# Optimization experiments

Measured on AMD Instinct MI355X. Metric: run time of the kernel, lower is better.

Reference implementation:

```python
import jax, jax.numpy as jnp
import numpy as np

N_SRC = 50000
N_DST = 50000
N_EDGE = 800000
D_SRC = 128
D_DST = 128
D_EDGE = D_SRC + 2 + D_DST  # 258


def setup_inputs() -> dict:
    key = jax.random.key(0)
    ks = jax.random.split(key, 7)
    return {
        "src_node_features": jax.random.normal(ks[0], (N_SRC, D_SRC), jnp.float32),
        "edge_src_idx": jax.random.randint(ks[1], (N_EDGE,), 0, N_SRC, dtype=jnp.int32),
        "dst_node_features": jax.random.normal(ks[2], (N_DST, D_DST), jnp.float32),
        "edge_dst_idx": jax.random.randint(ks[3], (N_EDGE,), 0, N_DST, dtype=jnp.int32),
        "edge_dist_rel": jax.random.normal(ks[4], (N_EDGE, 2), jnp.float32),
        # nn.Linear(258, 1, bias=False) weight stored as a [258] vector
        "w_att": jax.random.normal(ks[5], (D_EDGE,), jnp.float32) * 0.05,
        # nn.Linear(258, 128, bias=False) weight stored transposed [258, 128]
        "w_embed": jax.random.normal(ks[6], (D_EDGE, D_DST), jnp.float32) * 0.05,
    }


def reference(src_node_features, edge_src_idx, dst_node_features, edge_dst_idx,
              edge_dist_rel, w_att, w_embed):
    # Gather endpoint features per edge and concat with relative distance: [E, 258]
    x = jnp.concatenate([
        src_node_features[edge_src_idx],
        edge_dist_rel,
        dst_node_features[edge_dst_idx],
    ], axis=-1)

    # Edge attention score: Linear(258->1, no bias) + LeakyReLU(0.2)
    score = x @ w_att                                     # [E]
    score = jnp.where(score >= 0, score, 0.2 * score)

    # scatter_softmax over destination segments (numerically stable)
    seg_max = jax.ops.segment_max(score, edge_dst_idx, num_segments=N_DST)
    seg_max = jnp.where(jnp.isfinite(seg_max), seg_max, 0.0)  # empty segments
    e = jnp.exp(score - seg_max[edge_dst_idx])
    denom = jax.ops.segment_sum(e, edge_dst_idx, num_segments=N_DST)
    attn = e / denom[edge_dst_idx]                        # [E]
    # Dropout is identity in eval mode.

    # Edge embedding and attention-weighted scatter_add: [N_DST, 128]
    emb = x @ w_embed                                     # [E, 128]
    out = jax.ops.segment_sum(attn[:, None] * emb, edge_dst_idx, num_segments=N_DST)
    return jax.nn.relu(out)
```

## Files before the change

kernel.cpp:

```cpp
#include <hip/hip_runtime.h>
#include <hip/hip_bf16.h>

#define D 128
#define NPB 64
#define EPB1 2048
#define BDST 32
#define CAP 1024
#define MAXBINS 2048
#define NCHUNK 8

typedef __attribute__((ext_vector_type(8))) short short8;
typedef __attribute__((ext_vector_type(4))) float f32x4;

static __device__ __forceinline__ unsigned short f32_to_bf16(float f) {
    unsigned int u = __float_as_uint(f);
    u = (u + 0x7FFFu + ((u >> 16) & 1u)) >> 16;
    return (unsigned short)u;
}
static __device__ __forceinline__ float bf16lo(unsigned int r) {
    return __uint_as_float(r << 16);
}
static __device__ __forceinline__ float bf16hi(unsigned int r) {
    return __uint_as_float(r & 0xFFFF0000u);
}

__global__ void __launch_bounds__(256)
wconv_kernel(const float* __restrict__ w_embed, unsigned short* __restrict__ w_frag)
{
    int t = blockIdx.x * 256 + threadIdx.x;
    if (t >= 4096) return;
    int set  = t >> 11;
    int ks   = (t >> 9) & 3;
    int nt   = (t >> 6) & 7;
    int lane = t & 63;
    int wrow0 = set ? 130 : 0;
    int col   = nt * 16 + (lane & 15);
    int kbase = ks * 32 + (lane >> 4) * 8;
    unsigned short* dst = w_frag + (size_t)t * 8;
#pragma unroll
    for (int j = 0; j < 8; ++j)
        dst[j] = f32_to_bf16(w_embed[(size_t)(wrow0 + kbase + j) * D + col]);
}

__global__ void __launch_bounds__(256)
proj_both_kernel(const float* __restrict__ src_feat, const float* __restrict__ dst_feat,
                 const unsigned short* __restrict__ wfrag_base,
                 const float* __restrict__ w_att,
                 int n_src, int n_dst, int nblk_src,
                 unsigned short* __restrict__ srcp, unsigned short* __restrict__ dstp,
                 float* __restrict__ src_att, float* __restrict__ dst_att)
{
    const bool is_src = (blockIdx.x < nblk_src);
    const float* feats = is_src ? src_feat : dst_feat;
    const unsigned short* wfrag = is_src ? wfrag_base : wfrag_base + 16384;
    const int wrow = is_src ? 0 : 130;
    const int n_nodes = is_src ? n_src : n_dst;
    unsigned short* proj = is_src ? srcp : dstp;
    float* att = is_src ? src_att : dst_att;
    const int blk = is_src ? blockIdx.x : blockIdx.x - nblk_src;

    __shared__ unsigned short s_tile[NPB * D];
    __shared__ float s_red[NPB][4];

    const int tid = threadIdx.x;
    const int node0 = blk * NPB;

#pragma unroll
    for (int it = 0; it < 8; ++it) {
        int idx = it * 256 + tid;
        int row = idx >> 5, c4 = idx & 31;
        int n = node0 + row;
        float4 v = (n < n_nodes)
                 ? *reinterpret_cast<const float4*>(&feats[(size_t)n * D + c4 * 4])
                 : make_float4(0.f, 0.f, 0.f, 0.f);
        unsigned short h[4];
        h[0] = f32_to_bf16(v.x); h[1] = f32_to_bf16(v.y);
        h[2] = f32_to_bf16(v.z); h[3] = f32_to_bf16(v.w);
        int byte = row * 256 + c4 * 8;
        byte ^= (row & 7) << 4;
        *reinterpret_cast<ushort4*>((char*)s_tile + byte) = *reinterpret_cast<ushort4*>(h);
    }
    __syncthreads();

    const int wv = tid >> 6, lane = tid & 63;

    f32x4 acc[8];
#pragma unroll
    for (int i = 0; i < 8; ++i) acc[i] = {0.f, 0.f, 0.f, 0.f};

    const int arow = wv * 16 + (lane & 15);
#pragma unroll
    for (int ks = 0; ks < 4; ++ks) {
        int abyte = arow * 256 + ks * 64 + (lane >> 4) * 16;
        abyte ^= (arow & 7) << 4;
        short8 a = *reinterpret_cast<const short8*>((char*)s_tile + abyte);
#pragma unroll
        for (int nt = 0; nt < 8; ++nt) {
            short8 b = *reinterpret_cast<const short8*>(wfrag + ((size_t)(ks * 8 + nt) * 64 + lane) * 8);
            acc[nt] = __builtin_amdgcn_mfma_f32_16x16x32_bf16(a, b, acc[nt], 0, 0, 0);
        }
    }

#pragma unroll
    for (int nt = 0; nt < 8; ++nt) {
#pragma unroll
        for (int r = 0; r < 4; ++r) {
            int node = node0 + wv * 16 + (lane >> 4) * 4 + r;
            if (node < n_nodes)
                proj[(size_t)node * D + nt * 16 + (lane & 15)] = f32_to_bf16(acc[nt][r]);
        }
    }

    const int na = tid & 63, kq = tid >> 6;
    float p = 0.f;
#pragma unroll
    for (int k = kq * 32; k < kq * 32 + 32; ++k) {
        int byte = (na * 256 + k * 2) ^ ((na & 7) << 4);
        unsigned short h = *reinterpret_cast<const unsigned short*>((char*)s_tile + byte);
        p += __uint_as_float(((unsigned int)h) << 16) * w_att[wrow + k];
    }
    s_red[na][kq] = p;
    __syncthreads();
    if (tid < NPB) {
        int n = node0 + tid;
        if (n < n_nodes)
            att[n] = s_red[tid][0] + s_red[tid][1] + s_red[tid][2] + s_red[tid][3];
    }
}

__global__ void __launch_bounds__(512)
hist1_kernel(const int* __restrict__ edst, int* __restrict__ bb,
             int n_edge, int nblk1, int nb1)
{
    __shared__ int bins[MAXBINS];
    const int tid = threadIdx.x, blk = blockIdx.x;
    for (int i = tid; i < nb1; i += 512) bins[i] = 0;
    __syncthreads();
    const int e0 = blk * EPB1 + tid * 4;
    if (e0 + 4 <= n_edge) {
        int4 d4 = *reinterpret_cast<const int4*>(&edst[e0]);
        atomicAdd(&bins[((unsigned)d4.x) >> 5], 1);
        atomicAdd(&bins[((unsigned)d4.y) >> 5], 1);
        atomicAdd(&bins[((unsigned)d4.z) >> 5], 1);
        atomicAdd(&bins[((unsigned)d4.w) >> 5], 1);
    } else {
        for (int e = e0; e < n_edge; ++e)
            atomicAdd(&bins[((unsigned)edst[e]) >> 5], 1);
    }
    __syncthreads();
    for (int i = tid; i < nb1; i += 512) bb[(size_t)blk * nb1 + i] = bins[i];
}

__global__ void __launch_bounds__(256)
chunksum_kernel(const int* __restrict__ bb, int* __restrict__ cs,
                int nb1, int nblk1, int cb)
{
    int t = blockIdx.x * 256 + threadIdx.x;
    if (t >= nb1 * NCHUNK) return;
    int c = t / nb1, bin = t - c * nb1;
    int b0 = c * cb, b1 = min(b0 + cb, nblk1);
    int s = 0;
    for (int blk = b0; blk < b1; ++blk)
        s += bb[(size_t)blk * nb1 + bin];
    cs[(size_t)c * nb1 + bin] = s;
}

__global__ void __launch_bounds__(1024)
midscan_kernel(int* __restrict__ cs, int* __restrict__ binstart,
               int nb1, int n_edge)
{
    __shared__ int s_tot[MAXBINS];
    __shared__ int s_w[16];
    __shared__ int s_total;
    __shared__ int s_carry;
    const int tid = threadIdx.x;
    const int lane = tid & 63, wid = tid >> 6;

    for (int bin = tid; bin < nb1; bin += 1024) {
        int run = 0;
#pragma unroll
        for (int c = 0; c < NCHUNK; ++c) {
            size_t idx = (size_t)c * nb1 + bin;
            int v = cs[idx];
            cs[idx] = run;
            run += v;
        }
        s_tot[bin] = run;
    }
    if (tid == 0) s_carry = 0;
    __syncthreads();

    for (int base = 0; base < nb1; base += 1024) {
        int idx = base + tid;
        int v = (idx < nb1) ? s_tot[idx] : 0;
        int x = v;
#pragma unroll
        for (int off = 1; off < 64; off <<= 1) {
            int y = __shfl_up(x, off);
            if (lane >= off) x += y;
        }
        if (lane == 63) s_w[wid] = x;
        __syncthreads();
        if (tid < 16) {
            int w = s_w[tid];
            int xi = w;
#pragma unroll
            for (int off = 1; off < 16; off <<= 1) {
                int y = __shfl_up(xi, off);
                if (tid >= off) xi += y;
            }
            if (tid == 15) s_total = xi;
            s_w[tid] = xi - w;
        }
        __syncthreads();
        if (idx < nb1) binstart[idx] = s_carry + s_w[wid] + (x - v);
        __syncthreads();
        if (tid == 0) s_carry += s_total;
        __syncthreads();
    }
    if (tid == 0) binstart[nb1] = n_edge;
}

__global__ void __launch_bounds__(256)
chunkwrite_kernel(int* __restrict__ bb, const int* __restrict__ cs,
                  int nb1, int nblk1, int cb)
{
    int t = blockIdx.x * 256 + threadIdx.x;
    if (t >= nb1 * NCHUNK) return;
    int c = t / nb1, bin = t - c * nb1;
    int b0 = c * cb, b1 = min(b0 + cb, nblk1);
    int carry = cs[(size_t)c * nb1 + bin];
    for (int blk0 = b0; blk0 < b1; blk0 += 8) {
        int v[8];
#pragma unroll
        for (int j = 0; j < 8; ++j) {
            int blk = blk0 + j;
            v[j] = (blk < b1) ? bb[(size_t)blk * nb1 + bin] : 0;
        }
#pragma unroll
        for (int j = 0; j < 8; ++j) {
            int blk = blk0 + j;
            if (blk < b1) bb[(size_t)blk * nb1 + bin] = carry;
            carry += v[j];
        }
    }
}

__global__ void __launch_bounds__(512)
pass1_kernel(const int* __restrict__ esrc, const int* __restrict__ edst,
             const float* __restrict__ dist,
             const float* __restrict__ src_att, const float* __restrict__ dst_att,
             const float* __restrict__ w_att,
             const int* __restrict__ bb, const int* __restrict__ binstart,
             float4* __restrict__ meta1, int n_edge, int nblk1, int nb1)
{
    __shared__ int cur[MAXBINS];
    const int tid = threadIdx.x, blk = blockIdx.x;
    for (int i = tid; i < nb1; i += 512)
        cur[i] = binstart[i] + bb[(size_t)blk * nb1 + i];
    __syncthreads();

    const float wa0 = w_att[128], wa1 = w_att[129];
    const int e0 = blk * EPB1 + tid * 4;
    if (e0 + 4 <= n_edge) {
        int4 s4 = *reinterpret_cast<const int4*>(&esrc[e0]);
        int4 d4 = *reinterpret_cast<const int4*>(&edst[e0]);
        float4 da = *reinterpret_cast<const float4*>(&dist[2 * (size_t)e0]);
        float4 db = *reinterpret_cast<const float4*>(&dist[2 * (size_t)e0 + 4]);
        float sa0 = src_att[s4.x], sa1 = src_att[s4.y];
        float sa2 = src_att[s4.z], sa3 = src_att[s4.w];
        float ta0 = dst_att[d4.x], ta1 = dst_att[d4.y];
        float ta2 = dst_att[d4.z], ta3 = dst_att[d4.w];
        float c0 = sa0 + ta0 + da.x * wa0 + da.y * wa1;
        float c1 = sa1 + ta1 + da.z * wa0 + da.w * wa1;
        float c2 = sa2 + ta2 + db.x * wa0 + db.y * wa1;
        float c3 = sa3 + ta3 + db.z * wa0 + db.w * wa1;
        c0 = (c0 >= 0.f) ? c0 : 0.2f * c0;
        c1 = (c1 >= 0.f) ? c1 : 0.2f * c1;
        c2 = (c2 >= 0.f) ? c2 : 0.2f * c2;
        c3 = (c3 >= 0.f) ? c3 : 0.2f * c3;
        float w0 = __expf(c0), w1 = __expf(c1), w2 = __expf(c2), w3 = __expf(c3);
        int p0 = atomicAdd(&cur[((unsigned)d4.x) >> 5], 1);
        int p1 = atomicAdd(&cur[((unsigned)d4.y) >> 5], 1);
        int p2 = atomicAdd(&cur[((unsigned)d4.z) >> 5], 1);
        int p3 = atomicAdd(&cur[((unsigned)d4.w) >> 5], 1);
        meta1[p0] = make_float4(__int_as_float(s4.x | ((d4.x & 31) << 24)), w0, da.x, da.y);
        meta1[p1] = make_float4(__int_as_float(s4.y | ((d4.y & 31) << 24)), w1, da.z, da.w);
        meta1[p2] = make_float4(__int_as_float(s4.z | ((d4.z & 31) << 24)), w2, db.x, db.y);
        meta1[p3] = make_float4(__int_as_float(s4.w | ((d4.w & 31) << 24)), w3, db.z, db.w);
    } else {
        for (int e = e0; e < n_edge; ++e) {
            int s = esrc[e];
            int d = edst[e];
            float2 dd = *reinterpret_cast<const float2*>(&dist[2 * (size_t)e]);
            float sc = src_att[s] + dst_att[d] + dd.x * wa0 + dd.y * wa1;
            sc = (sc >= 0.f) ? sc : 0.2f * sc;
            float ew = __expf(sc);
            int pos = atomicAdd(&cur[((unsigned)d) >> 5], 1);
            meta1[pos] = make_float4(__int_as_float(s | ((d & 31) << 24)), ew, dd.x, dd.y);
        }
    }
}

__global__ void __launch_bounds__(256)
p2agg_kernel(const float4* __restrict__ meta1, const int* __restrict__ binstart,
             const unsigned short* __restrict__ srcp,
             const unsigned short* __restrict__ dstp,
             const float* __restrict__ w_embed,
             float* __restrict__ out, int n_dst)
{
    __shared__ float4 s_meta[CAP];
    __shared__ int s_cnt[BDST];
    __shared__ int s_ofs[BDST + 1];
    __shared__ int s_cur[BDST];

    const int tid = threadIdx.x;
    const int b = blockIdx.x;
    const int bstart = binstart[b], bend = binstart[b + 1];
    const int bsize = bend - bstart;
    const int lane = tid & 63, wv = tid >> 6;
    const int c0 = 2 * lane;

    const float2 wd0 = *reinterpret_cast<const float2*>(&w_embed[128 * D + c0]);
    const float2 wd1 = *reinterpret_cast<const float2*>(&w_embed[129 * D + c0]);

    if (tid < BDST) s_cnt[tid] = 0;
    __syncthreads();

    if (bsize <= CAP) {
        for (int i = tid; i < bsize; i += 256) {
            int bits = __float_as_int(meta1[bstart + i].x);
            atomicAdd(&s_cnt[((unsigned)bits) >> 24], 1);
        }
        __syncthreads();
        if (tid < BDST) {
            int v = s_cnt[tid];
            int x = v;
#pragma unroll
            for (int off = 1; off < BDST; off <<= 1) {
                int y = __shfl_up(x, off);
                if (tid >= off) x += y;
            }
            s_ofs[tid] = x - v;
            s_cur[tid] = x - v;
            if (tid == BDST - 1) s_ofs[BDST] = x;
        }
        __syncthreads();
        for (int i = tid; i < bsize; i += 256) {
            float4 m = meta1[bstart + i];
            int dlow = ((unsigned)__float_as_int(m.x)) >> 24;
            int pos = atomicAdd(&s_cur[dlow], 1);
            s_meta[pos] = m;
        }
        __syncthreads();

#define EDGE_ACC(m)                                                               \
        {                                                                         \
            int bits_ = __float_as_int((m).x);                                    \
            unsigned int r_ = *reinterpret_cast<const unsigned int*>(             \
                &srcp[(size_t)(bits_ & 0xFFFFFF) * D + c0]);                      \
            acc0 += (m).y * bf16lo(r_);                                           \
            acc1 += (m).y * bf16hi(r_);                                           \
            sw   += (m).y;                                                        \
            swd0 += (m).y * (m).z;                                                \
            swd1 += (m).y * (m).w;                                                \
        }
#pragma unroll
        for (int k = 0; k < 8; ++k) {
            int dloc = k * 4 + wv;
            int gd = b * BDST + dloc;
            if (gd >= n_dst) continue;
            float2* op = reinterpret_cast<float2*>(&out[(size_t)gd * D + c0]);
            int o0 = s_ofs[dloc], o1 = s_ofs[dloc + 1];
            if (o0 == o1) { *op = make_float2(0.f, 0.f); continue; }

            float acc0 = 0.f, acc1 = 0.f, sw = 0.f, swd0 = 0.f, swd1 = 0.f;
            int j = o0;
            for (; j + 8 <= o1; j += 8) {
                float4 m0 = s_meta[j + 0];
                float4 m1 = s_meta[j + 1];
                float4 m2 = s_meta[j + 2];
                float4 m3 = s_meta[j + 3];
                float4 m4 = s_meta[j + 4];
                float4 m5 = s_meta[j + 5];
                float4 m6 = s_meta[j + 6];
                float4 m7 = s_meta[j + 7];
                EDGE_ACC(m0) EDGE_ACC(m1) EDGE_ACC(m2) EDGE_ACC(m3)
                EDGE_ACC(m4) EDGE_ACC(m5) EDGE_ACC(m6) EDGE_ACC(m7)
            }
            for (; j < o1; ++j) {
                float4 m0 = s_meta[j];
                EDGE_ACC(m0)
            }
            float inv = 1.f / sw;
            unsigned int rd = *reinterpret_cast<const unsigned int*>(&dstp[(size_t)gd * D + c0]);
            float ov0 = (acc0 + swd0 * wd0.x + swd1 * wd1.x) * inv + bf16lo(rd);
            float ov1 = (acc1 + swd0 * wd0.y + swd1 * wd1.y) * inv + bf16hi(rd);
            *op = make_float2(fmaxf(ov0, 0.f), fmaxf(ov1, 0.f));
        }
#undef EDGE_ACC
    } else {
        float acc0[8], acc1[8], sw[8], s0[8], s1[8];
        for (int k = 0; k < 8; ++k) { acc0[k] = acc1[k] = sw[k] = s0[k] = s1[k] = 0.f; }
        for (int cs2 = bstart; cs2 < bend; cs2 += CAP) {
            int n = min(CAP, bend - cs2);
            __syncthreads();
            for (int i = tid; i < n; i += 256) s_meta[i] = meta1[cs2 + i];
            __syncthreads();
            for (int k = 0; k < 8; ++k) {
                int dloc = k * 4 + wv;
                for (int i = 0; i < n; ++i) {
                    float4 m = s_meta[i];
                    int bits = __float_as_int(m.x);
                    if ((int)(((unsigned)bits) >> 24) == dloc) {
                        unsigned int r = *reinterpret_cast<const unsigned int*>(
                            &srcp[(size_t)(bits & 0xFFFFFF) * D + c0]);
                        acc0[k] += m.y * bf16lo(r);
                        acc1[k] += m.y * bf16hi(r);
                        sw[k] += m.y;
                        s0[k] += m.y * m.z;
                        s1[k] += m.y * m.w;
                    }
                }
            }
        }
        for (int k = 0; k < 8; ++k) {
            int dloc = k * 4 + wv;
            int gd = b * BDST + dloc;
            if (gd >= n_dst) continue;
            float2* op = reinterpret_cast<float2*>(&out[(size_t)gd * D + c0]);
            if (sw[k] == 0.f) { *op = make_float2(0.f, 0.f); continue; }
            float inv = 1.f / sw[k];
            unsigned int rd = *reinterpret_cast<const unsigned int*>(&dstp[(size_t)gd * D + c0]);
            float ov0 = (acc0[k] + s0[k] * wd0.x + s1[k] * wd1.x) * inv + bf16lo(rd);
            float ov1 = (acc1[k] + s0[k] * wd0.y + s1[k] * wd1.y) * inv + bf16hi(rd);
            *op = make_float2(fmaxf(ov0, 0.f), fmaxf(ov1, 0.f));
        }
    }
}

extern "C" void kernel_launch(void* const* d_in, const int* in_sizes, int n_in,
                              void* d_out, int out_size, void* d_ws, size_t ws_size,
                              hipStream_t stream)
{
    const float* src_feat = (const float*)d_in[0];
    const int*   esrc     = (const int*)d_in[1];
    const float* dst_feat = (const float*)d_in[2];
    const int*   edst     = (const int*)d_in[3];
    const float* dist     = (const float*)d_in[4];
    const float* w_att    = (const float*)d_in[5];
    const float* w_embed  = (const float*)d_in[6];

    const int n_src  = in_sizes[0] / D;
    const int n_edge = in_sizes[1];
    const int n_dst  = in_sizes[2] / D;

    const int nb1   = (n_dst + BDST - 1) / BDST;
    const int nblk1 = (n_edge + EPB1 - 1) / EPB1;
    const int cb    = (nblk1 + NCHUNK - 1) / NCHUNK;
    const size_t n1 = (size_t)nb1 * nblk1;

    char* p = (char*)d_ws;
    auto carve = [&p](size_t bytes) {
        char* r = p;
        p += (bytes + 255) & ~size_t(255);
        return r;
    };
    unsigned short* src_projb = (unsigned short*)carve((size_t)n_src * D * 2);
    unsigned short* dst_projb = (unsigned short*)carve((size_t)n_dst * D * 2);
    float* src_att   = (float*)carve((size_t)n_src * 4);
    float* dst_att   = (float*)carve((size_t)n_dst * 4);
    int*   bb        = (int*)carve(n1 * 4);
    int*   cs        = (int*)carve((size_t)NCHUNK * nb1 * 4);
    int*   binstart  = (int*)carve((size_t)(nb1 + 1) * 4);
    unsigned short* w_frag = (unsigned short*)carve(2 * 4 * 8 * 64 * 8 * 2);
    float4* meta1    = (float4*)carve((size_t)n_edge * 16);
    (void)ws_size;

    wconv_kernel<<<16, 256, 0, stream>>>(w_embed, w_frag);

    const int nblk_src = (n_src + NPB - 1) / NPB;
    const int nblk_dst = (n_dst + NPB - 1) / NPB;
    proj_both_kernel<<<nblk_src + nblk_dst, 256, 0, stream>>>(
        src_feat, dst_feat, w_frag, w_att, n_src, n_dst, nblk_src,
        src_projb, dst_projb, src_att, dst_att);

    hist1_kernel<<<nblk1, 512, 0, stream>>>(edst, bb, n_edge, nblk1, nb1);

    const int nthr_cs = nb1 * NCHUNK;
    chunksum_kernel<<<(nthr_cs + 255) / 256, 256, 0, stream>>>(bb, cs, nb1, nblk1, cb);
    midscan_kernel<<<1, 1024, 0, stream>>>(cs, binstart, nb1, n_edge);
    chunkwrite_kernel<<<(nthr_cs + 255) / 256, 256, 0, stream>>>(bb, cs, nb1, nblk1, cb);

    pass1_kernel<<<nblk1, 512, 0, stream>>>(esrc, edst, dist, src_att, dst_att,
                                            w_att, bb, binstart, meta1,
                                            n_edge, nblk1, nb1);

    p2agg_kernel<<<nb1, 256, 0, stream>>>(meta1, binstart, src_projb, dst_projb,
                                          w_embed, (float*)d_out, n_dst);
}
```

Measured before the change: 113.9 us.

## Stage gathered source rows in LDS chunks with cooperative 16-byte loads

The aggregation kernel now cooperatively gathers chunks of 64 source-feature rows into shared memory using 16-byte loads per thread, then each wave accumulates its destinations from LDS. The per-destination weight sums are computed up front with a wave-parallel reduction instead of serially per edge. This is meant to replace per-lane 4-byte scattered global loads with wider coalesced loads. In exchange it adds a block-wide barrier per chunk, extra LDS use that may lower occupancy, and serial per-destination loops over each chunk that leave most waves idle when few of their edges fall in a chunk.

```diff
diff --git a/kernel.cpp b/kernel.cpp
--- a/kernel.cpp
+++ b/kernel.cpp
@@ -8,6 +8,7 @@
 #define CAP 1024
 #define MAXBINS 2048
 #define NCHUNK 8
+#define NC 64
 
 typedef __attribute__((ext_vector_type(8))) short short8;
 typedef __attribute__((ext_vector_type(4))) float f32x4;
@@ -310,6 +311,7 @@
              float* __restrict__ out, int n_dst)
 {
     __shared__ float4 s_meta[CAP];
+    __shared__ unsigned short s_rows[NC * D];
     __shared__ int s_cnt[BDST];
     __shared__ int s_ofs[BDST + 1];
     __shared__ int s_cur[BDST];
@@ -354,51 +356,69 @@
         }
         __syncthreads();
 
-#define EDGE_ACC(m)                                                               \
-        {                                                                         \
-            int bits_ = __float_as_int((m).x);                                    \
-            unsigned int r_ = *reinterpret_cast<const unsigned int*>(             \
-                &srcp[(size_t)(bits_ & 0xFFFFFF) * D + c0]);                      \
-            acc0 += (m).y * bf16lo(r_);                                           \
-            acc1 += (m).y * bf16hi(r_);                                           \
-            sw   += (m).y;                                                        \
-            swd0 += (m).y * (m).z;                                                \
-            swd1 += (m).y * (m).w;                                                \
-        }
+        int o0[8], o1[8];
+        float sw[8], sd0[8], sd1[8];
+#pragma unroll
+        for (int k = 0; k < 8; ++k) {
+            int dloc = k * 4 + wv;
+            o0[k] = s_ofs[dloc];
+            o1[k] = s_ofs[dloc + 1];
+            float a = 0.f, p = 0.f, q = 0.f;
+            for (int j = o0[k] + lane; j < o1[k]; j += 64) {
+                float4 m = s_meta[j];
+                a += m.y; p += m.y * m.z; q += m.y * m.w;
+            }
+#pragma unroll
+            for (int off = 32; off > 0; off >>= 1) {
+                a += __shfl_xor(a, off);
+                p += __shfl_xor(p, off);
+                q += __shfl_xor(q, off);
+            }
+            sw[k] = a; sd0[k] = p; sd1[k] = q;
+        }
+
+        float a0[8], a1[8];
+#pragma unroll
+        for (int k = 0; k < 8; ++k) { a0[k] = 0.f; a1[k] = 0.f; }
+
+        for (int cb2 = 0; cb2 < bsize; cb2 += NC) {
+            const int nrows = min(NC, bsize - cb2);
+            __syncthreads();
+            for (int i = tid; i < nrows * 16; i += 256) {
+                int r = i >> 4, seg = i & 15;
+                int bits = __float_as_int(s_meta[cb2 + r].x);
+                *reinterpret_cast<float4*>(&s_rows[r * D + seg * 8]) =
+                    *reinterpret_cast<const float4*>(
+                        &srcp[(size_t)(bits & 0xFFFFFF) * D + seg * 8]);
+            }
+            __syncthreads();
+            const int ce = cb2 + nrows;
+#pragma unroll
+            for (int k = 0; k < 8; ++k) {
+                int j0 = max(o0[k], cb2), j1 = min(o1[k], ce);
+                for (int j = j0; j < j1; ++j) {
+                    float at = s_meta[j].y;
+                    unsigned int r_ = *reinterpret_cast<const unsigned int*>(
+                        &s_rows[(j - cb2) * D + c0]);
+                    a0[k] += at * bf16lo(r_);
+                    a1[k] += at * bf16hi(r_);
+                }
+            }
+        }
+
 #pragma unroll
         for (int k = 0; k < 8; ++k) {
             int dloc = k * 4 + wv;
             int gd = b * BDST + dloc;
             if (gd >= n_dst) continue;
             float2* op = reinterpret_cast<float2*>(&out[(size_t)gd * D + c0]);
-            int o0 = s_ofs[dloc], o1 = s_ofs[dloc + 1];
-            if (o0 == o1) { *op = make_float2(0.f, 0.f); continue; }
-
-            float acc0 = 0.f, acc1 = 0.f, sw = 0.f, swd0 = 0.f, swd1 = 0.f;
-            int j = o0;
-            for (; j + 8 <= o1; j += 8) {
-                float4 m0 = s_meta[j + 0];
-                float4 m1 = s_meta[j + 1];
-                float4 m2 = s_meta[j + 2];
-                float4 m3 = s_meta[j + 3];
-                float4 m4 = s_meta[j + 4];
-                float4 m5 = s_meta[j + 5];
-                float4 m6 = s_meta[j + 6];
-                float4 m7 = s_meta[j + 7];
-                EDGE_ACC(m0) EDGE_ACC(m1) EDGE_ACC(m2) EDGE_ACC(m3)
-                EDGE_ACC(m4) EDGE_ACC(m5) EDGE_ACC(m6) EDGE_ACC(m7)
-            }
-            for (; j < o1; ++j) {
-                float4 m0 = s_meta[j];
-                EDGE_ACC(m0)
-            }
-            float inv = 1.f / sw;
+            if (o0[k] == o1[k]) { *op = make_float2(0.f, 0.f); continue; }
+            float inv = 1.f / sw[k];
             unsigned int rd = *reinterpret_cast<const unsigned int*>(&dstp[(size_t)gd * D + c0]);
-            float ov0 = (acc0 + swd0 * wd0.x + swd1 * wd1.x) * inv + bf16lo(rd);
-            float ov1 = (acc1 + swd0 * wd0.y + swd1 * wd1.y) * inv + bf16hi(rd);
+            float ov0 = (a0[k] + sd0[k] * wd0.x + sd1[k] * wd1.x) * inv + bf16lo(rd);
+            float ov1 = (a1[k] + sd0[k] * wd0.y + sd1[k] * wd1.y) * inv + bf16hi(rd);
             *op = make_float2(fmaxf(ov0, 0.f), fmaxf(ov1, 0.f));
         }
-#undef EDGE_ACC
     } else {
         float acc0[8], acc1[8], sw[8], s0[8], s1[8];
         for (int k = 0; k < 8; ++k) { acc0[k] = acc1[k] = sw[k] = s0[k] = s1[k] = 0.f; }
```

Result: slower. 146.6 us (+28.7%).

## Process four edges per wave with 16-byte row loads and cross-lane reduction

Applied to the files above, without the earlier changes.

In the aggregation kernel's fast path, each wave now splits into four groups of 16 lanes. Each group handles a different edge, and each lane loads 8 bf16 features (16 bytes) at once, instead of one 4-byte load per lane per edge across all 64 lanes. Partial sums are combined with xor shuffles before one group writes the output row. The aim is more memory-level parallelism and fewer load instructions on the gather. The cost is shuffle reductions and wasted lanes on the tail iterations when a destination has few edges.

```diff
diff --git a/kernel.cpp b/kernel.cpp
--- a/kernel.cpp
+++ b/kernel.cpp
@@ -319,10 +319,8 @@
     const int bstart = binstart[b], bend = binstart[b + 1];
     const int bsize = bend - bstart;
     const int lane = tid & 63, wv = tid >> 6;
-    const int c0 = 2 * lane;
-
-    const float2 wd0 = *reinterpret_cast<const float2*>(&w_embed[128 * D + c0]);
-    const float2 wd1 = *reinterpret_cast<const float2*>(&w_embed[129 * D + c0]);
+    const int eg = lane >> 4;
+    const int sg = lane & 15;
 
     if (tid < BDST) s_cnt[tid] = 0;
     __syncthreads();
@@ -354,52 +352,88 @@
         }
         __syncthreads();
 
-#define EDGE_ACC(m)                                                               \
-        {                                                                         \
-            int bits_ = __float_as_int((m).x);                                    \
-            unsigned int r_ = *reinterpret_cast<const unsigned int*>(             \
-                &srcp[(size_t)(bits_ & 0xFFFFFF) * D + c0]);                      \
-            acc0 += (m).y * bf16lo(r_);                                           \
-            acc1 += (m).y * bf16hi(r_);                                           \
-            sw   += (m).y;                                                        \
-            swd0 += (m).y * (m).z;                                                \
-            swd1 += (m).y * (m).w;                                                \
-        }
+        const float4 wr0a = *reinterpret_cast<const float4*>(&w_embed[128 * D + sg * 8]);
+        const float4 wr0b = *reinterpret_cast<const float4*>(&w_embed[128 * D + sg * 8 + 4]);
+        const float4 wr1a = *reinterpret_cast<const float4*>(&w_embed[129 * D + sg * 8]);
+        const float4 wr1b = *reinterpret_cast<const float4*>(&w_embed[129 * D + sg * 8 + 4]);
+
 #pragma unroll
         for (int k = 0; k < 8; ++k) {
-            int dloc = k * 4 + wv;
-            int gd = b * BDST + dloc;
+            const int dloc = k * 4 + wv;
+            const int gd = b * BDST + dloc;
             if (gd >= n_dst) continue;
-            float2* op = reinterpret_cast<float2*>(&out[(size_t)gd * D + c0]);
-            int o0 = s_ofs[dloc], o1 = s_ofs[dloc + 1];
-            if (o0 == o1) { *op = make_float2(0.f, 0.f); continue; }
-
-            float acc0 = 0.f, acc1 = 0.f, sw = 0.f, swd0 = 0.f, swd1 = 0.f;
-            int j = o0;
-            for (; j + 8 <= o1; j += 8) {
-                float4 m0 = s_meta[j + 0];
-                float4 m1 = s_meta[j + 1];
-                float4 m2 = s_meta[j + 2];
-                float4 m3 = s_meta[j + 3];
-                float4 m4 = s_meta[j + 4];
-                float4 m5 = s_meta[j + 5];
-                float4 m6 = s_meta[j + 6];
-                float4 m7 = s_meta[j + 7];
-                EDGE_ACC(m0) EDGE_ACC(m1) EDGE_ACC(m2) EDGE_ACC(m3)
-                EDGE_ACC(m4) EDGE_ACC(m5) EDGE_ACC(m6) EDGE_ACC(m7)
-            }
-            for (; j < o1; ++j) {
-                float4 m0 = s_meta[j];
-                EDGE_ACC(m0)
-            }
-            float inv = 1.f / sw;
-            unsigned int rd = *reinterpret_cast<const unsigned int*>(&dstp[(size_t)gd * D + c0]);
-            float ov0 = (acc0 + swd0 * wd0.x + swd1 * wd1.x) * inv + bf16lo(rd);
-            float ov1 = (acc1 + swd0 * wd0.y + swd1 * wd1.y) * inv + bf16hi(rd);
-            *op = make_float2(fmaxf(ov0, 0.f), fmaxf(ov1, 0.f));
-        }
-#undef EDGE_ACC
+            const int o0 = s_ofs[dloc], o1 = s_ofs[dloc + 1];
+            float* orow = &out[(size_t)gd * D];
+            if (o0 == o1) {
+                if (eg == 0) {
+                    *reinterpret_cast<float4*>(&orow[sg * 8]) = make_float4(0.f, 0.f, 0.f, 0.f);
+                    *reinterpret_cast<float4*>(&orow[sg * 8 + 4]) = make_float4(0.f, 0.f, 0.f, 0.f);
+                }
+                continue;
+            }
+
+            float a0 = 0.f, a1 = 0.f, a2 = 0.f, a3 = 0.f;
+            float a4 = 0.f, a5 = 0.f, a6 = 0.f, a7 = 0.f;
+            float psw = 0.f, psd0 = 0.f, psd1 = 0.f;
+
+            for (int j0 = o0; j0 < o1; j0 += 4) {
+                int j = j0 + eg;
+                bool valid = (j < o1);
+                float4 m = s_meta[valid ? j : o0];
+                float at = valid ? m.y : 0.f;
+                int src = __float_as_int(m.x) & 0xFFFFFF;
+                float4 r = *reinterpret_cast<const float4*>(
+                    &srcp[(size_t)src * D + sg * 8]);
+                unsigned int r0 = __float_as_uint(r.x);
+                unsigned int r1 = __float_as_uint(r.y);
+                unsigned int r2 = __float_as_uint(r.z);
+                unsigned int r3 = __float_as_uint(r.w);
+                a0 += at * bf16lo(r0); a1 += at * bf16hi(r0);
+                a2 += at * bf16lo(r1); a3 += at * bf16hi(r1);
+                a4 += at * bf16lo(r2); a5 += at * bf16hi(r2);
+                a6 += at * bf16lo(r3); a7 += at * bf16hi(r3);
+                if (sg == 0) {
+                    psw += at; psd0 += at * m.z; psd1 += at * m.w;
+                }
+            }
+
+#pragma unroll
+            for (int off = 16; off < 64; off <<= 1) {
+                a0 += __shfl_xor(a0, off); a1 += __shfl_xor(a1, off);
+                a2 += __shfl_xor(a2, off); a3 += __shfl_xor(a3, off);
+                a4 += __shfl_xor(a4, off); a5 += __shfl_xor(a5, off);
+                a6 += __shfl_xor(a6, off); a7 += __shfl_xor(a7, off);
+                psw += __shfl_xor(psw, off);
+                psd0 += __shfl_xor(psd0, off);
+                psd1 += __shfl_xor(psd1, off);
+            }
+            const float sw  = __shfl(psw, 0);
+            const float sd0 = __shfl(psd0, 0);
+            const float sd1 = __shfl(psd1, 0);
+
+            if (eg == 0) {
+                const float inv = 1.f / sw;
+                unsigned int d0 = *reinterpret_cast<const unsigned int*>(&dstp[(size_t)gd * D + sg * 8]);
+                unsigned int d1 = *reinterpret_cast<const unsigned int*>(&dstp[(size_t)gd * D + sg * 8 + 2]);
+                unsigned int d2 = *reinterpret_cast<const unsigned int*>(&dstp[(size_t)gd * D + sg * 8 + 4]);
+                unsigned int d3 = *reinterpret_cast<const unsigned int*>(&dstp[(size_t)gd * D + sg * 8 + 6]);
+                float4 oA, oB;
+                oA.x = fmaxf((a0 + sd0 * wr0a.x + sd1 * wr1a.x) * inv + bf16lo(d0), 0.f);
+                oA.y = fmaxf((a1 + sd0 * wr0a.y + sd1 * wr1a.y) * inv + bf16hi(d0), 0.f);
+                oA.z = fmaxf((a2 + sd0 * wr0a.z + sd1 * wr1a.z) * inv + bf16lo(d1), 0.f);
+                oA.w = fmaxf((a3 + sd0 * wr0a.w + sd1 * wr1a.w) * inv + bf16hi(d1), 0.f);
+                oB.x = fmaxf((a4 + sd0 * wr0b.x + sd1 * wr1b.x) * inv + bf16lo(d2), 0.f);
+                oB.y = fmaxf((a5 + sd0 * wr0b.y + sd1 * wr1b.y) * inv + bf16hi(d2), 0.f);
+                oB.z = fmaxf((a6 + sd0 * wr0b.z + sd1 * wr1b.z) * inv + bf16lo(d3), 0.f);
+                oB.w = fmaxf((a7 + sd0 * wr0b.w + sd1 * wr1b.w) * inv + bf16hi(d3), 0.f);
+                *reinterpret_cast<float4*>(&orow[sg * 8]) = oA;
+                *reinterpret_cast<float4*>(&orow[sg * 8 + 4]) = oB;
+            }
+        }
     } else {
+        const int c0 = 2 * lane;
+        const float2 wd0 = *reinterpret_cast<const float2*>(&w_embed[128 * D + c0]);
+        const float2 wd1 = *reinterpret_cast<const float2*>(&w_embed[129 * D + c0]);
         float acc0[8], acc1[8], sw[8], s0[8], s1[8];
         for (int k = 0; k < 8; ++k) { acc0[k] = acc1[k] = sw[k] = s0[k] = s1[k] = 0.f; }
         for (int cs2 = bstart; cs2 < bend; cs2 += CAP) {
```

After: 112.7 us (median of 2 runs). Within noise of the previous version (-1.0%).
